# Optimization experiments

Hardware: AMD Instinct MI355X
Metric: run time of the kernel (lower is better)

Reference implementation:

```python
import jax, jax.numpy as jnp
import numpy as np

LORA_SCALING = 1.0 / 2.0  # lora_alpha / lora_r = 1/2


def _qlora_linear(x, wq, A, B):
    # wq: (out, in/4) fake-NF4 compressed weight, repeated x4 -> (out, in)
    w = jnp.tile(wq, (1, 4))
    base = x @ w.T                              # (..., out)
    lora = (x @ A.T) @ B.T                      # low-rank path, r=2
    return base + lora * LORA_SCALING


def setup_inputs() -> dict:
    key = jax.random.key(0)
    ks = jax.random.split(key, 10)
    d, h, r = 4096, 11008, 2
    return {
        "x":   jax.random.normal(ks[0], (16, 1, d), dtype=jnp.float32),
        "w1q": jax.random.normal(ks[1], (h, d // 4), dtype=jnp.float32) * 0.02,
        "a1":  jax.random.normal(ks[2], (r, d), dtype=jnp.float32) * 0.02,
        "b1":  jax.random.normal(ks[3], (h, r), dtype=jnp.float32) * 0.02,
        "w3q": jax.random.normal(ks[4], (h, d // 4), dtype=jnp.float32) * 0.02,
        "a3":  jax.random.normal(ks[5], (r, d), dtype=jnp.float32) * 0.02,
        "b3":  jax.random.normal(ks[6], (h, r), dtype=jnp.float32) * 0.02,
        "w2q": jax.random.normal(ks[7], (d, h // 4), dtype=jnp.float32) * 0.02,
        "a2":  jax.random.normal(ks[8], (r, h), dtype=jnp.float32) * 0.02,
        "b2":  jax.random.normal(ks[9], (d, r), dtype=jnp.float32) * 0.02,
    }


def reference(x, w1q, a1, b1, w3q, a3, b3, w2q, a2, b2):
    # SwiGLU MLP: w2( silu(w1(x)) * w3(x) ), each linear = repeat-dequant + LoRA
    gate = jax.nn.silu(_qlora_linear(x, w1q, a1, b1))  # (B, S, hidden)
    up = _qlora_linear(x, w3q, a3, b3)                 # (B, S, hidden)
    return _qlora_linear(gate * up, w2q, a2, b2)       # (B, S, d_model)
```

## Files before the change

### kernel.cpp

```cpp
#include <hip/hip_runtime.h>
#include <hip/hip_bf16.h>


#define NB     16
#define DMODEL 4096
#define HID    11008
#define DQ     1024
#define HQ     2752

#define XSB_OFF 0
#define T1_OFF  8192
#define T3_OFF  8224
#define HF_OFF  8256
#define T2_OFF  52288

typedef __attribute__((ext_vector_type(8))) short bf16x8;
typedef __attribute__((ext_vector_type(4))) float f32x4;

__device__ __forceinline__ unsigned short f2bfh(float f) {
  __hip_bfloat16 h = __float2bfloat16(f);
  return __builtin_bit_cast(unsigned short, h);
}
__device__ __forceinline__ unsigned pack2(float lo, float hi) {
  return (unsigned)f2bfh(lo) | ((unsigned)f2bfh(hi) << 16);
}
__device__ __forceinline__ bf16x8 cvt8(const float4 a, const float4 b) {
  uint4 u = make_uint4(pack2(a.x, a.y), pack2(a.z, a.w),
                       pack2(b.x, b.y), pack2(b.z, b.w));
  return __builtin_bit_cast(bf16x8, u);
}

__global__ __launch_bounds__(256) void k_prep1(const float* __restrict__ x,
                                               const float* __restrict__ a1,
                                               const float* __restrict__ a3,
                                               float* __restrict__ ws,
                                               float* __restrict__ out) {
  const int b = blockIdx.x, t = threadIdx.x;
  const int gid = b * 256 + t;
  const float4 z4 = make_float4(0.f, 0.f, 0.f, 0.f);
  for (int i = gid; i < 11016; i += 4096)
    ((float4*)(ws + HF_OFF))[i] = z4;
  for (int i = gid; i < 16384; i += 4096)
    ((float4*)out)[i] = z4;

  const float4* x4  = (const float4*)(x) + b * (DMODEL / 4);
  const float4* a14 = (const float4*)a1;
  const float4* a34 = (const float4*)a3;
  float4 xs = z4;
  float s10 = 0.f, s11 = 0.f, s30 = 0.f, s31 = 0.f;
#pragma unroll
  for (int k = 0; k < 4; ++k) {
    float4 xv  = x4[k * 256 + t];
    xs.x += xv.x; xs.y += xv.y; xs.z += xv.z; xs.w += xv.w;
    float4 a10 = a14[k * 256 + t];
    float4 a11 = a14[1024 + k * 256 + t];
    float4 a30 = a34[k * 256 + t];
    float4 a31 = a34[1024 + k * 256 + t];
    s10 += xv.x * a10.x + xv.y * a10.y + xv.z * a10.z + xv.w * a10.w;
    s11 += xv.x * a11.x + xv.y * a11.y + xv.z * a11.z + xv.w * a11.w;
    s30 += xv.x * a30.x + xv.y * a30.y + xv.z * a30.z + xv.w * a30.w;
    s31 += xv.x * a31.x + xv.y * a31.y + xv.z * a31.z + xv.w * a31.w;
  }
  ((uint2*)(ws + XSB_OFF))[b * 256 + t] =
      make_uint2(pack2(xs.x, xs.y), pack2(xs.z, xs.w));

  __shared__ float4 rb[256];
  rb[t] = make_float4(s10, s11, s30, s31);
  __syncthreads();
  for (int s = 128; s > 0; s >>= 1) {
    if (t < s) {
      rb[t].x += rb[t + s].x; rb[t].y += rb[t + s].y;
      rb[t].z += rb[t + s].z; rb[t].w += rb[t + s].w;
    }
    __syncthreads();
  }
  if (t == 0) {
    ws[T1_OFF + b * 2]     = rb[0].x;
    ws[T1_OFF + b * 2 + 1] = rb[0].y;
    ws[T3_OFF + b * 2]     = rb[0].z;
    ws[T3_OFF + b * 2 + 1] = rb[0].w;
  }
}

#define GU_PF(KK, W1A, W1B, W3A, W3B, XB) do {                              \
    const int _ka = k0 + (KK) * 32 + kb;                                    \
    const float4* _p1 = (const float4*)(w1q + (size_t)o * DQ + _ka);        \
    const float4* _p3 = (const float4*)(w3q + (size_t)o * DQ + _ka);        \
    W1A = _p1[0]; W1B = _p1[1];                                             \
    W3A = _p3[0]; W3B = _p3[1];                                             \
    XB  = *(const bf16x8*)(xsb + n * DQ + _ka);                             \
  } while (0)

#define GU_MM(W1A, W1B, W3A, W3B, XB) do {                                  \
    acc1 = __builtin_amdgcn_mfma_f32_16x16x32_bf16(cvt8(W1A, W1B), XB,      \
                                                   acc1, 0, 0, 0);          \
    acc3 = __builtin_amdgcn_mfma_f32_16x16x32_bf16(cvt8(W3A, W3B), XB,      \
                                                   acc3, 0, 0, 0);          \
  } while (0)

#define SB __builtin_amdgcn_sched_barrier(0)

__global__ __launch_bounds__(256) void k_gateup(const float* __restrict__ w1q,
                                                const float* __restrict__ w3q,
                                                const float* __restrict__ b1,
                                                const float* __restrict__ b3,
                                                const float* __restrict__ a2,
                                                float* __restrict__ ws) {
  __shared__ float red[4][8][64];
  const int t = threadIdx.x, w = t >> 6, l = t & 63;
  const int tile = blockIdx.x;
  const int n  = l & 15;
  const int kb = (l >> 4) * 8;
  const int o  = tile * 16 + n;
  const int k0 = w * 256;
  const unsigned short* xsb = (const unsigned short*)(ws + XSB_OFF);

  f32x4 acc1 = {0.f, 0.f, 0.f, 0.f}, acc3 = {0.f, 0.f, 0.f, 0.f};

  float4 p0a, p0b, q0a, q0b;  bf16x8 x0;
  float4 p1a, p1b, q1a, q1b;  bf16x8 x1;
  float4 p2a, p2b, q2a, q2b;  bf16x8 x2;
  float4 p3a, p3b, q3a, q3b;  bf16x8 x3;

  GU_PF(0, p0a, p0b, q0a, q0b, x0);
  GU_PF(1, p1a, p1b, q1a, q1b, x1);
  GU_PF(2, p2a, p2b, q2a, q2b, x2);
  GU_PF(3, p3a, p3b, q3a, q3b, x3);
  SB;
  GU_MM(p0a, p0b, q0a, q0b, x0);  GU_PF(4, p0a, p0b, q0a, q0b, x0);  SB;
  GU_MM(p1a, p1b, q1a, q1b, x1);  GU_PF(5, p1a, p1b, q1a, q1b, x1);  SB;
  GU_MM(p2a, p2b, q2a, q2b, x2);  GU_PF(6, p2a, p2b, q2a, q2b, x2);  SB;
  GU_MM(p3a, p3b, q3a, q3b, x3);  GU_PF(7, p3a, p3b, q3a, q3b, x3);  SB;
  GU_MM(p0a, p0b, q0a, q0b, x0);
  GU_MM(p1a, p1b, q1a, q1b, x1);
  GU_MM(p2a, p2b, q2a, q2b, x2);
  GU_MM(p3a, p3b, q3a, q3b, x3);

#pragma unroll
  for (int r = 0; r < 4; ++r) {
    red[w][r][l]     = acc1[r];
    red[w][r + 4][l] = acc3[r];
  }
  __syncthreads();
  if (w == 0) {
    const float t10 = ws[T1_OFF + 2 * n], t11 = ws[T1_OFF + 2 * n + 1];
    const float t30 = ws[T3_OFF + 2 * n], t31 = ws[T3_OFF + 2 * n + 1];
    const int m4 = (l >> 4) * 4;
    float s0 = 0.f, s1 = 0.f;
#pragma unroll
    for (int r = 0; r < 4; ++r) {
      float g0 = 0.f, u0 = 0.f;
#pragma unroll
      for (int ww = 0; ww < 4; ++ww) {
        g0 += red[ww][r][l];
        u0 += red[ww][r + 4][l];
      }
      const int oo = tile * 16 + m4 + r;
      const float g = g0 + 0.5f * (t10 * b1[2 * oo] + t11 * b1[2 * oo + 1]);
      const float u = u0 + 0.5f * (t30 * b3[2 * oo] + t31 * b3[2 * oo + 1]);
      const float v = (g / (1.f + __expf(-g))) * u;
      atomicAdd(&ws[HF_OFF + n * HQ + (oo % HQ)], v);
      s0 += v * a2[oo];
      s1 += v * a2[HID + oo];
    }
    s0 += __shfl_xor(s0, 16);  s0 += __shfl_xor(s0, 32);
    s1 += __shfl_xor(s1, 16);  s1 += __shfl_xor(s1, 32);
    if (l < 16) {
      atomicAdd(&ws[T2_OFF + 2 * n], s0);
      atomicAdd(&ws[T2_OFF + 2 * n + 1], s1);
    }
  }
}

#define DN_PF(KK, WA, WB, HA, HB) do {                                      \
    const int _ka = (kks + (KK)) * 32 + kb;                                 \
    const float4* _p2 = (const float4*)(w2q + (size_t)o * HQ + _ka);        \
    const float4* _pb = (const float4*)(hf + (size_t)n * HQ + _ka);         \
    WA = _p2[0]; WB = _p2[1]; HA = _pb[0]; HB = _pb[1];                     \
  } while (0)

#define DN_MM(WA, WB, HA, HB)                                               \
  acc = __builtin_amdgcn_mfma_f32_16x16x32_bf16(cvt8(WA, WB),               \
                                                cvt8(HA, HB), acc, 0, 0, 0)

__global__ __launch_bounds__(256) void k_down(const float* __restrict__ w2q,
                                              const float* __restrict__ b2,
                                              const float* __restrict__ ws,
                                              float* __restrict__ out) {
  __shared__ float red[4][4][64];
  const int t = threadIdx.x, w = t >> 6, l = t & 63;
  const int tile = blockIdx.x >> 1, half = blockIdx.x & 1;
  const int g = half * 4 + w;
  const int n  = l & 15;
  const int kb = (l >> 4) * 8;
  const int o  = tile * 16 + n;
  const float* hf = ws + HF_OFF;
  const int kks  = (g < 6) ? g * 11 : 66 + (g - 6) * 10;
  const int klen = (g < 6) ? 11 : 10;

  f32x4 acc = {0.f, 0.f, 0.f, 0.f};
  float4 w0a, w0b, h0a, h0b;
  float4 w1a, w1b, h1a, h1b;
  float4 w2a, w2b, h2a, h2b;
  float4 w3a, w3b, h3a, h3b;

  DN_PF(0, w0a, w0b, h0a, h0b);
  DN_PF(1, w1a, w1b, h1a, h1b);
  DN_PF(2, w2a, w2b, h2a, h2b);
  DN_PF(3, w3a, w3b, h3a, h3b);
  SB;
  DN_MM(w0a, w0b, h0a, h0b);  DN_PF(4, w0a, w0b, h0a, h0b);  SB;
  DN_MM(w1a, w1b, h1a, h1b);  DN_PF(5, w1a, w1b, h1a, h1b);  SB;
  DN_MM(w2a, w2b, h2a, h2b);  DN_PF(6, w2a, w2b, h2a, h2b);  SB;
  DN_MM(w3a, w3b, h3a, h3b);  DN_PF(7, w3a, w3b, h3a, h3b);  SB;
  DN_MM(w0a, w0b, h0a, h0b);  DN_PF(8, w0a, w0b, h0a, h0b);  SB;
  DN_MM(w1a, w1b, h1a, h1b);  DN_PF(9, w1a, w1b, h1a, h1b);  SB;
  DN_MM(w2a, w2b, h2a, h2b);
  if (klen > 10) { DN_PF(10, w2a, w2b, h2a, h2b); }
  SB;
  DN_MM(w3a, w3b, h3a, h3b);
  DN_MM(w0a, w0b, h0a, h0b);
  DN_MM(w1a, w1b, h1a, h1b);
  if (klen > 10) { DN_MM(w2a, w2b, h2a, h2b); }

#pragma unroll
  for (int r = 0; r < 4; ++r) red[w][r][l] = acc[r];
  __syncthreads();
  if (w == 0) {
    const float t20 = ws[T2_OFF + 2 * n], t21 = ws[T2_OFF + 2 * n + 1];
    const int m4 = (l >> 4) * 4;
#pragma unroll
    for (int r = 0; r < 4; ++r) {
      float v = red[0][r][l] + red[1][r][l] + red[2][r][l] + red[3][r][l];
      const int oo = tile * 16 + m4 + r;
      if (half == 0)
        v += 0.5f * (t20 * b2[2 * oo] + t21 * b2[2 * oo + 1]);
      atomicAdd(&out[n * DMODEL + oo], v);
    }
  }
}

extern "C" void kernel_launch(void* const* d_in, const int* in_sizes, int n_in,
                              void* d_out, int out_size, void* d_ws, size_t ws_size,
                              hipStream_t stream) {
  const float* x   = (const float*)d_in[0];
  const float* w1q = (const float*)d_in[1];
  const float* a1  = (const float*)d_in[2];
  const float* b1  = (const float*)d_in[3];
  const float* w3q = (const float*)d_in[4];
  const float* a3  = (const float*)d_in[5];
  const float* b3  = (const float*)d_in[6];
  const float* w2q = (const float*)d_in[7];
  const float* a2  = (const float*)d_in[8];
  const float* b2  = (const float*)d_in[9];
  float* out = (float*)d_out;
  float* ws  = (float*)d_ws;

  k_prep1<<<16, 256, 0, stream>>>(x, a1, a3, ws, out);
  k_gateup<<<HID / 16, 256, 0, stream>>>(w1q, w3q, b1, b3, a2, ws);
  k_down<<<2 * (DMODEL / 16), 256, 0, stream>>>(w2q, b2, ws, out);
}
```

Before: 53.80 us.

## Stage gate/up weight tiles through padded LDS with coalesced loads

The gate/up kernel now loads each 16-row by 256-column chunk of w1q and w3q into padded shared memory with fully coalesced float4 reads, then each wave feeds MFMA from LDS. Previously each lane read 32-byte strided pieces straight from global memory with a manual register prefetch pipeline. The prep kernel also grows to 64 blocks so the zeroing of the workspace and output is spread out, with one store per thread. The cost is two barriers per chunk and the loss of load/compute overlap, since the software prefetch pipeline is removed.

```diff
diff --git a/kernel.cpp b/kernel.cpp
--- a/kernel.cpp
+++ b/kernel.cpp
@@ -14,6 +14,8 @@
 #define HF_OFF  8256
 #define T2_OFF  52288
 
+#define LPAD 260
+
 typedef __attribute__((ext_vector_type(8))) short bf16x8;
 typedef __attribute__((ext_vector_type(4))) float f32x4;
 
@@ -35,14 +37,14 @@
                                                const float* __restrict__ a3,
                                                float* __restrict__ ws,
                                                float* __restrict__ out) {
-  const int b = blockIdx.x, t = threadIdx.x;
-  const int gid = b * 256 + t;
+  const int t = threadIdx.x;
+  const int gid = blockIdx.x * 256 + t;
   const float4 z4 = make_float4(0.f, 0.f, 0.f, 0.f);
-  for (int i = gid; i < 11016; i += 4096)
-    ((float4*)(ws + HF_OFF))[i] = z4;
-  for (int i = gid; i < 16384; i += 4096)
-    ((float4*)out)[i] = z4;
-
+  if (gid < 11016) ((float4*)(ws + HF_OFF))[gid] = z4;
+  ((float4*)out)[gid] = z4;
+  if (blockIdx.x >= 16) return;
+
+  const int b = blockIdx.x;
   const float4* x4  = (const float4*)(x) + b * (DMODEL / 4);
   const float4* a14 = (const float4*)a1;
   const float4* a34 = (const float4*)a3;
@@ -82,64 +84,56 @@
   }
 }
 
-#define GU_PF(KK, W1A, W1B, W3A, W3B, XB) do {                              \
-    const int _ka = k0 + (KK) * 32 + kb;                                    \
-    const float4* _p1 = (const float4*)(w1q + (size_t)o * DQ + _ka);        \
-    const float4* _p3 = (const float4*)(w3q + (size_t)o * DQ + _ka);        \
-    W1A = _p1[0]; W1B = _p1[1];                                             \
-    W3A = _p3[0]; W3B = _p3[1];                                             \
-    XB  = *(const bf16x8*)(xsb + n * DQ + _ka);                             \
-  } while (0)
-
-#define GU_MM(W1A, W1B, W3A, W3B, XB) do {                                  \
-    acc1 = __builtin_amdgcn_mfma_f32_16x16x32_bf16(cvt8(W1A, W1B), XB,      \
-                                                   acc1, 0, 0, 0);          \
-    acc3 = __builtin_amdgcn_mfma_f32_16x16x32_bf16(cvt8(W3A, W3B), XB,      \
-                                                   acc3, 0, 0, 0);          \
-  } while (0)
-
-#define SB __builtin_amdgcn_sched_barrier(0)
-
 __global__ __launch_bounds__(256) void k_gateup(const float* __restrict__ w1q,
                                                 const float* __restrict__ w3q,
                                                 const float* __restrict__ b1,
                                                 const float* __restrict__ b3,
                                                 const float* __restrict__ a2,
                                                 float* __restrict__ ws) {
-  __shared__ float red[4][8][64];
+  __shared__ float smem[2 * 16 * LPAD];
   const int t = threadIdx.x, w = t >> 6, l = t & 63;
-  const int tile = blockIdx.x;
+  const int row0 = blockIdx.x * 16;
   const int n  = l & 15;
   const int kb = (l >> 4) * 8;
-  const int o  = tile * 16 + n;
-  const int k0 = w * 256;
   const unsigned short* xsb = (const unsigned short*)(ws + XSB_OFF);
 
   f32x4 acc1 = {0.f, 0.f, 0.f, 0.f}, acc3 = {0.f, 0.f, 0.f, 0.f};
 
-  float4 p0a, p0b, q0a, q0b;  bf16x8 x0;
-  float4 p1a, p1b, q1a, q1b;  bf16x8 x1;
-  float4 p2a, p2b, q2a, q2b;  bf16x8 x2;
-  float4 p3a, p3b, q3a, q3b;  bf16x8 x3;
-
-  GU_PF(0, p0a, p0b, q0a, q0b, x0);
-  GU_PF(1, p1a, p1b, q1a, q1b, x1);
-  GU_PF(2, p2a, p2b, q2a, q2b, x2);
-  GU_PF(3, p3a, p3b, q3a, q3b, x3);
-  SB;
-  GU_MM(p0a, p0b, q0a, q0b, x0);  GU_PF(4, p0a, p0b, q0a, q0b, x0);  SB;
-  GU_MM(p1a, p1b, q1a, q1b, x1);  GU_PF(5, p1a, p1b, q1a, q1b, x1);  SB;
-  GU_MM(p2a, p2b, q2a, q2b, x2);  GU_PF(6, p2a, p2b, q2a, q2b, x2);  SB;
-  GU_MM(p3a, p3b, q3a, q3b, x3);  GU_PF(7, p3a, p3b, q3a, q3b, x3);  SB;
-  GU_MM(p0a, p0b, q0a, q0b, x0);
-  GU_MM(p1a, p1b, q1a, q1b, x1);
-  GU_MM(p2a, p2b, q2a, q2b, x2);
-  GU_MM(p3a, p3b, q3a, q3b, x3);
-
+  for (int c = 0; c < 4; ++c) {
+#pragma unroll
+    for (int it = 0; it < 8; ++it) {
+      const int i = it * 256 + t;
+      const int m = i >> 10, rem = i & 1023;
+      const int row = rem >> 6, col = rem & 63;
+      const float* src = m ? w3q : w1q;
+      const float4 v = *(const float4*)(src + (size_t)(row0 + row) * DQ +
+                                        c * 256 + col * 4);
+      *(float4*)(smem + m * (16 * LPAD) + row * LPAD + col * 4) = v;
+    }
+    __syncthreads();
+#pragma unroll
+    for (int j = 0; j < 2; ++j) {
+      const int kloc = (w * 2 + j) * 32 + kb;
+      const float* a1p = smem + n * LPAD + kloc;
+      const float* a3p = smem + 16 * LPAD + n * LPAD + kloc;
+      const float4 a1a = *(const float4*)(a1p);
+      const float4 a1b = *(const float4*)(a1p + 4);
+      const float4 a3a = *(const float4*)(a3p);
+      const float4 a3b = *(const float4*)(a3p + 4);
+      const bf16x8 bb = *(const bf16x8*)(xsb + n * DQ + c * 256 + kloc);
+      acc1 = __builtin_amdgcn_mfma_f32_16x16x32_bf16(cvt8(a1a, a1b), bb,
+                                                     acc1, 0, 0, 0);
+      acc3 = __builtin_amdgcn_mfma_f32_16x16x32_bf16(cvt8(a3a, a3b), bb,
+                                                     acc3, 0, 0, 0);
+    }
+    __syncthreads();
+  }
+
+  float* red = smem;
 #pragma unroll
   for (int r = 0; r < 4; ++r) {
-    red[w][r][l]     = acc1[r];
-    red[w][r + 4][l] = acc3[r];
+    red[(w * 8 + r) * 64 + l]     = acc1[r];
+    red[(w * 8 + r + 4) * 64 + l] = acc3[r];
   }
   __syncthreads();
   if (w == 0) {
@@ -152,10 +146,10 @@
       float g0 = 0.f, u0 = 0.f;
 #pragma unroll
       for (int ww = 0; ww < 4; ++ww) {
-        g0 += red[ww][r][l];
-        u0 += red[ww][r + 4][l];
+        g0 += red[(ww * 8 + r) * 64 + l];
+        u0 += red[(ww * 8 + r + 4) * 64 + l];
       }
-      const int oo = tile * 16 + m4 + r;
+      const int oo = row0 + m4 + r;
       const float g = g0 + 0.5f * (t10 * b1[2 * oo] + t11 * b1[2 * oo + 1]);
       const float u = u0 + 0.5f * (t30 * b3[2 * oo] + t31 * b3[2 * oo + 1]);
       const float v = (g / (1.f + __expf(-g))) * u;
@@ -171,6 +165,8 @@
     }
   }
 }
+
+#define SB __builtin_amdgcn_sched_barrier(0)
 
 #define DN_PF(KK, WA, WB, HA, HB) do {                                      \
     const int _ka = (kks + (KK)) * 32 + kb;                                 \
@@ -256,7 +252,7 @@
   float* out = (float*)d_out;
   float* ws  = (float*)d_ws;
 
-  k_prep1<<<16, 256, 0, stream>>>(x, a1, a3, ws, out);
+  k_prep1<<<64, 256, 0, stream>>>(x, a1, a3, ws, out);
   k_gateup<<<HID / 16, 256, 0, stream>>>(w1q, w3q, b1, b3, a2, ws);
   k_down<<<2 * (DMODEL / 16), 256, 0, stream>>>(w2q, b2, ws, out);
 }
```

New measurement: 62.33 us. 15.9% more time.
